# Kernel tuning notes

Hardware: AMD Instinct MI355X
Metric: run time of the kernel (lower is better)

The kernel has to match this reference:

```python
import jax, jax.numpy as jnp
import numpy as np

W_DIM = 512   # latent dim
CH = 512      # number of Fourier channels / output channels
SIZE = 64     # spatial size (square: size[0]=size[1])
SR = 64.0     # sampling_rate
BW = 2.0      # bandwidth
BATCH = 32


def setup_inputs() -> dict:
    key = jax.random.key(0)
    k1, k2, k3, k4, k5 = jax.random.split(key, 5)
    w = jax.random.normal(k1, (BATCH, W_DIM), jnp.float32)
    # affine FC params (weight_init=0 in original; use small random so t varies)
    affine_w = jax.random.normal(k2, (4, W_DIM), jnp.float32) * 0.1
    affine_b = jnp.array([1.0, 0.0, 0.0, 0.0], jnp.float32)
    # channel-mixing weight
    weight = jax.random.normal(k3, (CH, CH), jnp.float32)
    # freqs buffer init: randn, normalized by r*exp(r^2/4), scaled by bandwidth
    f = jax.random.normal(k4, (CH, 2), jnp.float32)
    radii = jnp.sqrt(jnp.sum(f * f, axis=1, keepdims=True))
    f = f / (radii * jnp.exp(radii * radii / 4.0)) * BW
    phases = jax.random.uniform(k5, (CH,), jnp.float32) - 0.5
    return {"w": w, "affine_w": affine_w, "affine_b": affine_b,
            "weight": weight, "freqs": f, "phases": phases}


def reference(w, affine_w, affine_b, weight, freqs, phases):
    # affine FC: FullyConnectedLayer with lr_multiplier=1 -> weight_gain = 1/sqrt(in)
    gain = np.float32(1.0 / np.sqrt(W_DIM))
    t = w @ (affine_w.T * gain) + affine_b                      # [N, 4]
    t = t / jnp.linalg.norm(t[:, :2], axis=1, keepdims=True)
    c, s, tx, ty = t[:, 0], t[:, 1], t[:, 2], t[:, 3]
    # combined transform = m_r @ m_t @ I; top-left 2x2 rotation block:
    R = jnp.stack([jnp.stack([c, -s], -1),
                   jnp.stack([s, c], -1)], axis=1)              # [N, 2, 2]
    # translation column of combined transform (m_r @ m_t)[:, :2, 2]
    trans = jnp.stack([-c * tx + s * ty, -s * tx - c * ty], -1) # [N, 2]
    ph = phases[None, :] + jnp.einsum('cd,nd->nc', freqs, trans)  # [N, C]
    fr = jnp.einsum('cd,nde->nce', freqs, R)                      # [N, C, 2]
    amp = jnp.clip(1.0 - (jnp.linalg.norm(fr, axis=2) - BW) / (SR / 2.0 - BW), 0.0, 1.0)  # [N, C]
    # affine_grid(theta, [1,1,H,W], align_corners=False): base coords (2i+1)/D - 1
    scale = np.float32(0.5 * SIZE / SR)
    xs = ((2.0 * jnp.arange(SIZE, dtype=jnp.float32) + 1.0) / SIZE - 1.0) * scale
    ys = ((2.0 * jnp.arange(SIZE, dtype=jnp.float32) + 1.0) / SIZE - 1.0) * scale
    grid = jnp.stack([jnp.broadcast_to(xs[None, :], (SIZE, SIZE)),
                      jnp.broadcast_to(ys[:, None], (SIZE, SIZE))], axis=-1)  # [H, W, 2]
    # per-pixel Fourier phase: [N, H, W, C]
    x = jnp.einsum('hwd,ncd->nhwc', grid, fr) + ph[:, None, None, :]
    x = jnp.sin(x * np.float32(2.0 * np.pi)) * amp[:, None, None, :]
    # channel projection, then to NCHW
    x = jnp.einsum('nhwc,kc->nkhw', x, weight * np.float32(1.0 / np.sqrt(CH)))
    return x  # [N, CH, H, W]
```

## Files before the change

### kernel.cpp

```cpp
#include <hip/hip_runtime.h>
#include <hip/hip_bf16.h>

#define WDIM 512
#define CHN  512
#define NB   32
#define SZ   64
#define MTOT 4096

typedef __attribute__((ext_vector_type(4))) float f32x4;
typedef __attribute__((ext_vector_type(8))) short short8;
typedef __attribute__((ext_vector_type(4))) int   int4v;
typedef __attribute__((ext_vector_type(4))) unsigned int uint4v;

__device__ __forceinline__ unsigned pack_bf(float a, float b) {
    union { __hip_bfloat16 h; unsigned short u; } x, y;
    x.h = __float2bfloat16(a); y.h = __float2bfloat16(b);
    return (unsigned)x.u | ((unsigned)y.u << 16);
}
__device__ __forceinline__ float lo16f(unsigned u) {
    union { unsigned x; float f; } t; t.x = u << 16; return t.f;
}
__device__ __forceinline__ float hi16f(unsigned u) {
    union { unsigned x; float f; } t; t.x = u & 0xffff0000u; return t.f;
}

__global__ __launch_bounds__(512) void prep_kernel(
    const float* __restrict__ win,
    const float* __restrict__ affine_w,
    const float* __restrict__ affine_b,
    const float* __restrict__ freqs,
    const float* __restrict__ phases,
    const float* __restrict__ wsrc,
    unsigned* __restrict__ SCA, unsigned* __restrict__ SCB,
    __hip_bfloat16* __restrict__ wbf)
{
    const int b = blockIdx.x;
    const int tid = threadIdx.x;
    if (b < NB * 64) {
        const int n = b >> 6;
        const int w = b & 63;
        __shared__ float red[8][4];
        __shared__ float par[4];

        float wv = win[n * WDIM + tid];
        float p0 = wv * affine_w[0 * WDIM + tid];
        float p1 = wv * affine_w[1 * WDIM + tid];
        float p2 = wv * affine_w[2 * WDIM + tid];
        float p3 = wv * affine_w[3 * WDIM + tid];
        #pragma unroll
        for (int off = 32; off >= 1; off >>= 1) {
            p0 += __shfl_down(p0, off);
            p1 += __shfl_down(p1, off);
            p2 += __shfl_down(p2, off);
            p3 += __shfl_down(p3, off);
        }
        const int wave = tid >> 6;
        if ((tid & 63) == 0) {
            red[wave][0] = p0; red[wave][1] = p1;
            red[wave][2] = p2; red[wave][3] = p3;
        }
        __syncthreads();
        if (tid == 0) {
            const float gain = 0.04419417382415922f;
            float t[4];
            #pragma unroll
            for (int j = 0; j < 4; ++j) {
                float s = 0.0f;
                #pragma unroll
                for (int v = 0; v < 8; ++v) s += red[v][j];
                t[j] = s * gain + affine_b[j];
            }
            float inv = 1.0f / sqrtf(t[0] * t[0] + t[1] * t[1]);
            float c = t[0] * inv, s = t[1] * inv, tx = t[2] * inv, ty = t[3] * inv;
            par[0] = c;
            par[1] = s;
            par[2] = -c * tx + s * ty;
            par[3] = -s * tx - c * ty;
        }
        __syncthreads();
        const float c_ = par[0], s_ = par[1], tr0 = par[2], tr1 = par[3];
        const int c = tid;
        float fx = freqs[c * 2 + 0], fy = freqs[c * 2 + 1];
        float frx = fx * c_ + fy * s_;
        float fry = -fx * s_ + fy * c_;
        float ph = phases[c] + fx * tr0 + fy * tr1;
        float r = sqrtf(frx * frx + fry * fry);
        float amp = 1.0f - (r - 2.0f) * (1.0f / 30.0f);
        amp = fminf(fmaxf(amp, 0.0f), 1.0f);
        float xs = (float)(2 * w + 1) * (1.0f / 128.0f) - 0.5f;
        size_t idx = ((size_t)(n * 64 + w)) * CHN + c;
        float sA = amp * __builtin_amdgcn_sinf(xs * frx);
        float cA = amp * __builtin_amdgcn_cosf(xs * frx);
        float bb = xs * fry + ph;
        SCA[idx] = pack_bf(sA, cA);
        SCB[idx] = pack_bf(__builtin_amdgcn_sinf(bb), __builtin_amdgcn_cosf(bb));
    } else {
        int i = (b - NB * 64) * 512 + tid;
        wbf[i] = __float2bfloat16(wsrc[i] * 0.04419417382415922f);
    }
}

__global__ __launch_bounds__(256, 2) void fused_kernel(
    const unsigned* __restrict__ SCA, const unsigned* __restrict__ SCB,
    const __hip_bfloat16* __restrict__ wbf,
    float* __restrict__ out)
{
    __shared__ __align__(16) __hip_bfloat16 As[128 * 64];
    __shared__ __align__(16) __hip_bfloat16 Bs[256 * 64];

    const int bid  = blockIdx.x;
    const int orig = (bid & 7) * 256 + (bid >> 3);
    const int n  = orig >> 6;
    const int kb = ((orig >> 5) & 1) * 256;
    const int mb = (orig & 31) * 128;
    const int h0 = mb >> 6;

    const int tid = threadIdx.x;
    const int lane = tid & 63;
    const int wid  = tid >> 6;
    const int ln15 = lane & 15;
    const int hi4  = lane >> 4;
    const int wk   = wid * 64;

    const int cc0 = (tid & 7) * 8;
    const int rb  = tid >> 3;

    const unsigned* pA0 = SCA + ((size_t)(n * 64 + rb)) * CHN + cc0;
    const unsigned* pA1 = pA0 + 32 * CHN;
    const unsigned* pB0 = SCB + ((size_t)(n * 64 + h0)) * CHN + cc0;
    const unsigned* pB1 = pB0 + CHN;

    f32x4 acc[4][8];
    #pragma unroll
    for (int a = 0; a < 4; ++a)
        #pragma unroll
        for (int b = 0; b < 8; ++b)
            acc[a][b] = (f32x4)0.0f;

    #pragma unroll 1
    for (int kc = 0; kc < 8; ++kc) {
        const int c0 = kc * 64;
        __syncthreads();

        #pragma unroll
        for (int u = 0; u < 8; ++u) {
            int unit = u * 256 + tid;
            int row = unit >> 3;
            int cbyte = ((unit & 7) << 4) ^ ((row & 7) << 4);
            const __hip_bfloat16* src = wbf + (size_t)(kb + row) * CHN + c0 + (cbyte >> 1);
            char* ldsbase = (char*)Bs + (u * 256 + (wid << 6)) * 16;
            __builtin_amdgcn_global_load_lds(
                (const __attribute__((address_space(1))) unsigned int*)src,
                (__attribute__((address_space(3))) unsigned int*)ldsbase, 16, 0, 0);
        }

        uint4v A00 = *(const uint4v*)(pA0 + c0), A01 = *(const uint4v*)(pA0 + c0 + 4);
        uint4v A10 = *(const uint4v*)(pA1 + c0), A11 = *(const uint4v*)(pA1 + c0 + 4);
        uint4v B00 = *(const uint4v*)(pB0 + c0), B01 = *(const uint4v*)(pB0 + c0 + 4);
        uint4v B10 = *(const uint4v*)(pB1 + c0), B11 = *(const uint4v*)(pB1 + c0 + 4);
        #pragma unroll
        for (int i = 0; i < 4; ++i) {
            int m = rb + i * 32;
            uint4v Aa = (i & 1) ? A10 : A00, Ab = (i & 1) ? A11 : A01;
            uint4v Ba = (i >> 1) ? B10 : B00, Bb = (i >> 1) ? B11 : B01;
            union { __hip_bfloat16 h[8]; int4v v; } t;
            #pragma unroll
            for (int j = 0; j < 4; ++j)
                t.h[j] = __float2bfloat16(
                    lo16f(Aa[j]) * hi16f(Ba[j]) + hi16f(Aa[j]) * lo16f(Ba[j]));
            #pragma unroll
            for (int j = 0; j < 4; ++j)
                t.h[4 + j] = __float2bfloat16(
                    lo16f(Ab[j]) * hi16f(Bb[j]) + hi16f(Ab[j]) * lo16f(Bb[j]));
            *(int4v*)((char*)As + m * 128 + ((cc0 * 2) ^ ((m & 7) << 4))) = t.v;
        }
        __syncthreads();

        #pragma unroll
        for (int kk = 0; kk < 2; ++kk) {
            short8 wf[4], ff[8];
            #pragma unroll
            for (int ki = 0; ki < 4; ++ki) {
                int row = wk + ki * 16 + ln15;
                wf[ki] = *(const short8*)((char*)Bs + row * 128 +
                          (((kk * 32 + hi4 * 8) * 2) ^ ((row & 7) << 4)));
            }
            #pragma unroll
            for (int mj = 0; mj < 8; ++mj) {
                int m = mj * 16 + ln15;
                ff[mj] = *(const short8*)((char*)As + m * 128 +
                          (((kk * 32 + hi4 * 8) * 2) ^ ((m & 7) << 4)));
            }
            __builtin_amdgcn_s_setprio(1);
            #pragma unroll
            for (int ki = 0; ki < 4; ++ki)
                #pragma unroll
                for (int mj = 0; mj < 8; ++mj)
                    acc[ki][mj] = __builtin_amdgcn_mfma_f32_16x16x32_bf16(
                        wf[ki], ff[mj], acc[ki][mj], 0, 0, 0);
            __builtin_amdgcn_s_setprio(0);
        }
    }

    #pragma unroll
    for (int ki = 0; ki < 4; ++ki) {
        #pragma unroll
        for (int mj = 0; mj < 8; ++mj) {
            int kg = kb + wk + ki * 16 + hi4 * 4;
            int mg = mb + mj * 16 + ln15;
            float* op = out + ((size_t)n * CHN + kg) * MTOT + mg;
            #pragma unroll
            for (int r = 0; r < 4; ++r)
                op[(size_t)r * MTOT] = acc[ki][mj][r];
        }
    }
}

extern "C" void kernel_launch(void* const* d_in, const int* in_sizes, int n_in,
                              void* d_out, int out_size, void* d_ws, size_t ws_size,
                              hipStream_t stream) {
    const float* w        = (const float*)d_in[0];
    const float* affine_w = (const float*)d_in[1];
    const float* affine_b = (const float*)d_in[2];
    const float* weight   = (const float*)d_in[3];
    const float* freqs    = (const float*)d_in[4];
    const float* phases   = (const float*)d_in[5];
    float* out = (float*)d_out;

    char* ws = (char*)d_ws;
    __hip_bfloat16* wbf = (__hip_bfloat16*)(ws);
    unsigned* SCA = (unsigned*)(ws + (1u << 20));
    unsigned* SCB = (unsigned*)(ws + (1u << 20) + (4u << 20));

    prep_kernel<<<NB * 64 + (CHN * CHN) / 512, 512, 0, stream>>>(
        w, affine_w, affine_b, freqs, phases, weight, SCA, SCB, wbf);

    fused_kernel<<<2048, 256, 0, stream>>>(SCA, SCB, wbf, out);
}
```

Before: 103.0 us.

## Warp-specialize fused GEMM into producer and consumer waves with double-buffered LDS

Result: slower. 121.1 us (+17.5%).

```diff
diff --git a/kernel.cpp b/kernel.cpp
--- a/kernel.cpp
+++ b/kernel.cpp
@@ -100,13 +100,13 @@
     }
 }
 
-__global__ __launch_bounds__(256, 2) void fused_kernel(
+__global__ __launch_bounds__(512, 2) void fused_kernel(
     const unsigned* __restrict__ SCA, const unsigned* __restrict__ SCB,
     const __hip_bfloat16* __restrict__ wbf,
     float* __restrict__ out)
 {
-    __shared__ __align__(16) __hip_bfloat16 As[128 * 64];
-    __shared__ __align__(16) __hip_bfloat16 Bs[256 * 64];
+    __shared__ __align__(16) __hip_bfloat16 As[2][128 * 64];
+    __shared__ __align__(16) __hip_bfloat16 Bs[2][256 * 64];
 
     const int bid  = blockIdx.x;
     const int orig = (bid & 7) * 256 + (bid >> 3);
@@ -116,102 +116,122 @@
     const int h0 = mb >> 6;
 
     const int tid = threadIdx.x;
-    const int lane = tid & 63;
-    const int wid  = tid >> 6;
-    const int ln15 = lane & 15;
-    const int hi4  = lane >> 4;
-    const int wk   = wid * 64;
-
-    const int cc0 = (tid & 7) * 8;
-    const int rb  = tid >> 3;
-
-    const unsigned* pA0 = SCA + ((size_t)(n * 64 + rb)) * CHN + cc0;
-    const unsigned* pA1 = pA0 + 32 * CHN;
-    const unsigned* pB0 = SCB + ((size_t)(n * 64 + h0)) * CHN + cc0;
-    const unsigned* pB1 = pB0 + CHN;
-
-    f32x4 acc[4][8];
-    #pragma unroll
-    for (int a = 0; a < 4; ++a)
+    const int wid = tid >> 6;
+    const bool producer = wid >= 4;
+
+    if (producer) {
+        const int ptid = tid - 256;
+        const int pwid = wid - 4;
+        const int cc0 = (ptid & 7) * 8;
+        const int rb  = ptid >> 3;
+
+        const unsigned* pA0 = SCA + ((size_t)(n * 64 + rb)) * CHN + cc0;
+        const unsigned* pA1 = pA0 + 32 * CHN;
+        const unsigned* pB0 = SCB + ((size_t)(n * 64 + h0)) * CHN + cc0;
+        const unsigned* pB1 = pB0 + CHN;
+
+        auto stageB = [&](int buf, int c0) {
+            #pragma unroll
+            for (int u = 0; u < 8; ++u) {
+                int unit = u * 256 + ptid;
+                int row = unit >> 3;
+                int cbyte = ((unit & 7) << 4) ^ ((row & 7) << 4);
+                const __hip_bfloat16* src = wbf + (size_t)(kb + row) * CHN + c0 + (cbyte >> 1);
+                char* ldsbase = (char*)Bs[buf] + (u * 256 + (pwid << 6)) * 16;
+                __builtin_amdgcn_global_load_lds(
+                    (const __attribute__((address_space(1))) unsigned int*)src,
+                    (__attribute__((address_space(3))) unsigned int*)ldsbase, 16, 0, 0);
+            }
+        };
+        auto features = [&](int buf, int c0) {
+            uint4v A00 = *(const uint4v*)(pA0 + c0), A01 = *(const uint4v*)(pA0 + c0 + 4);
+            uint4v A10 = *(const uint4v*)(pA1 + c0), A11 = *(const uint4v*)(pA1 + c0 + 4);
+            uint4v B00 = *(const uint4v*)(pB0 + c0), B01 = *(const uint4v*)(pB0 + c0 + 4);
+            uint4v B10 = *(const uint4v*)(pB1 + c0), B11 = *(const uint4v*)(pB1 + c0 + 4);
+            #pragma unroll
+            for (int i = 0; i < 4; ++i) {
+                int m = rb + i * 32;
+                uint4v Aa = (i & 1) ? A10 : A00, Ab = (i & 1) ? A11 : A01;
+                uint4v Ba = (i >> 1) ? B10 : B00, Bb = (i >> 1) ? B11 : B01;
+                union { __hip_bfloat16 h[8]; int4v v; } t;
+                #pragma unroll
+                for (int j = 0; j < 4; ++j)
+                    t.h[j] = __float2bfloat16(
+                        lo16f(Aa[j]) * hi16f(Ba[j]) + hi16f(Aa[j]) * lo16f(Ba[j]));
+                #pragma unroll
+                for (int j = 0; j < 4; ++j)
+                    t.h[4 + j] = __float2bfloat16(
+                        lo16f(Ab[j]) * hi16f(Bb[j]) + hi16f(Ab[j]) * lo16f(Bb[j]));
+                *(int4v*)((char*)As[buf] + m * 128 + ((cc0 * 2) ^ ((m & 7) << 4))) = t.v;
+            }
+        };
+
+        stageB(0, 0);
+        features(0, 0);
+        __syncthreads();
+        #pragma unroll 1
+        for (int kc = 0; kc < 8; ++kc) {
+            if (kc < 7) {
+                stageB((kc + 1) & 1, (kc + 1) * 64);
+                features((kc + 1) & 1, (kc + 1) * 64);
+            }
+            __syncthreads();
+        }
+    } else {
+        const int lane = tid & 63;
+        const int ln15 = lane & 15;
+        const int hi4  = lane >> 4;
+        const int wk   = wid * 64;
+
+        f32x4 acc[4][8];
         #pragma unroll
-        for (int b = 0; b < 8; ++b)
-            acc[a][b] = (f32x4)0.0f;
-
-    #pragma unroll 1
-    for (int kc = 0; kc < 8; ++kc) {
-        const int c0 = kc * 64;
-        __syncthreads();
+        for (int a = 0; a < 4; ++a)
+            #pragma unroll
+            for (int b = 0; b < 8; ++b)
+                acc[a][b] = (f32x4)0.0f;
+
+        __syncthreads();
+        #pragma unroll 1
+        for (int kc = 0; kc < 8; ++kc) {
+            const int buf = kc & 1;
+            #pragma unroll
+            for (int kk = 0; kk < 2; ++kk) {
+                short8 wf[4], ff[8];
+                #pragma unroll
+                for (int ki = 0; ki < 4; ++ki) {
+                    int row = wk + ki * 16 + ln15;
+                    wf[ki] = *(const short8*)((char*)Bs[buf] + row * 128 +
+                              (((kk * 32 + hi4 * 8) * 2) ^ ((row & 7) << 4)));
+                }
+                #pragma unroll
+                for (int mj = 0; mj < 8; ++mj) {
+                    int m = mj * 16 + ln15;
+                    ff[mj] = *(const short8*)((char*)As[buf] + m * 128 +
+                              (((kk * 32 + hi4 * 8) * 2) ^ ((m & 7) << 4)));
+                }
+                __builtin_amdgcn_s_setprio(1);
+                #pragma unroll
+                for (int ki = 0; ki < 4; ++ki)
+                    #pragma unroll
+                    for (int mj = 0; mj < 8; ++mj)
+                        acc[ki][mj] = __builtin_amdgcn_mfma_f32_16x16x32_bf16(
+                            wf[ki], ff[mj], acc[ki][mj], 0, 0, 0);
+                __builtin_amdgcn_s_setprio(0);
+            }
+            __syncthreads();
+        }
 
         #pragma unroll
-        for (int u = 0; u < 8; ++u) {
-            int unit = u * 256 + tid;
-            int row = unit >> 3;
-            int cbyte = ((unit & 7) << 4) ^ ((row & 7) << 4);
-            const __hip_bfloat16* src = wbf + (size_t)(kb + row) * CHN + c0 + (cbyte >> 1);
-            char* ldsbase = (char*)Bs + (u * 256 + (wid << 6)) * 16;
-            __builtin_amdgcn_global_load_lds(
-                (const __attribute__((address_space(1))) unsigned int*)src,
-                (__attribute__((address_space(3))) unsigned int*)ldsbase, 16, 0, 0);
-        }
-
-        uint4v A00 = *(const uint4v*)(pA0 + c0), A01 = *(const uint4v*)(pA0 + c0 + 4);
-        uint4v A10 = *(const uint4v*)(pA1 + c0), A11 = *(const uint4v*)(pA1 + c0 + 4);
-        uint4v B00 = *(const uint4v*)(pB0 + c0), B01 = *(const uint4v*)(pB0 + c0 + 4);
-        uint4v B10 = *(const uint4v*)(pB1 + c0), B11 = *(const uint4v*)(pB1 + c0 + 4);
-        #pragma unroll
-        for (int i = 0; i < 4; ++i) {
-            int m = rb + i * 32;
-            uint4v Aa = (i & 1) ? A10 : A00, Ab = (i & 1) ? A11 : A01;
-            uint4v Ba = (i >> 1) ? B10 : B00, Bb = (i >> 1) ? B11 : B01;
-            union { __hip_bfloat16 h[8]; int4v v; } t;
-            #pragma unroll
-            for (int j = 0; j < 4; ++j)
-                t.h[j] = __float2bfloat16(
-                    lo16f(Aa[j]) * hi16f(Ba[j]) + hi16f(Aa[j]) * lo16f(Ba[j]));
-            #pragma unroll
-            for (int j = 0; j < 4; ++j)
-                t.h[4 + j] = __float2bfloat16(
-                    lo16f(Ab[j]) * hi16f(Bb[j]) + hi16f(Ab[j]) * lo16f(Bb[j]));
-            *(int4v*)((char*)As + m * 128 + ((cc0 * 2) ^ ((m & 7) << 4))) = t.v;
-        }
-        __syncthreads();
-
-        #pragma unroll
-        for (int kk = 0; kk < 2; ++kk) {
-            short8 wf[4], ff[8];
-            #pragma unroll
-            for (int ki = 0; ki < 4; ++ki) {
-                int row = wk + ki * 16 + ln15;
-                wf[ki] = *(const short8*)((char*)Bs + row * 128 +
-                          (((kk * 32 + hi4 * 8) * 2) ^ ((row & 7) << 4)));
-            }
+        for (int ki = 0; ki < 4; ++ki) {
             #pragma unroll
             for (int mj = 0; mj < 8; ++mj) {
-                int m = mj * 16 + ln15;
-                ff[mj] = *(const short8*)((char*)As + m * 128 +
-                          (((kk * 32 + hi4 * 8) * 2) ^ ((m & 7) << 4)));
-            }
-            __builtin_amdgcn_s_setprio(1);
-            #pragma unroll
-            for (int ki = 0; ki < 4; ++ki)
-                #pragma unroll
-                for (int mj = 0; mj < 8; ++mj)
-                    acc[ki][mj] = __builtin_amdgcn_mfma_f32_16x16x32_bf16(
-                        wf[ki], ff[mj], acc[ki][mj], 0, 0, 0);
-            __builtin_amdgcn_s_setprio(0);
-        }
-    }
-
-    #pragma unroll
-    for (int ki = 0; ki < 4; ++ki) {
-        #pragma unroll
-        for (int mj = 0; mj < 8; ++mj) {
-            int kg = kb + wk + ki * 16 + hi4 * 4;
-            int mg = mb + mj * 16 + ln15;
-            float* op = out + ((size_t)n * CHN + kg) * MTOT + mg;
-            #pragma unroll
-            for (int r = 0; r < 4; ++r)
-                op[(size_t)r * MTOT] = acc[ki][mj][r];
+                int kg = kb + wk + ki * 16 + hi4 * 4;
+                int mg = mb + mj * 16 + ln15;
+                float* op = out + ((size_t)n * CHN + kg) * MTOT + mg;
+                #pragma unroll
+                for (int r = 0; r < 4; ++r)
+                    op[(size_t)r * MTOT] = acc[ki][mj][r];
+            }
         }
     }
 }
@@ -235,5 +255,5 @@
     prep_kernel<<<NB * 64 + (CHN * CHN) / 512, 512, 0, stream>>>(
         w, affine_w, affine_b, freqs, phases, weight, SCA, SCB, wbf);
 
-    fused_kernel<<<2048, 256, 0, stream>>>(SCA, SCB, wbf, out);
-}
+    fused_kernel<<<2048, 512, 0, stream>>>(SCA, SCB, wbf, out);
+}
```

## Load weights directly to registers and triple-buffer feature tiles in LDS

Applied to the files above, without the earlier changes.

Measured after the change: 127.7 us. 24.0% more time.

```diff
diff --git a/kernel.cpp b/kernel.cpp
--- a/kernel.cpp
+++ b/kernel.cpp
@@ -105,8 +105,7 @@
     const __hip_bfloat16* __restrict__ wbf,
     float* __restrict__ out)
 {
-    __shared__ __align__(16) __hip_bfloat16 As[128 * 64];
-    __shared__ __align__(16) __hip_bfloat16 Bs[256 * 64];
+    __shared__ __align__(16) __hip_bfloat16 As3[3][128 * 64];
 
     const int bid  = blockIdx.x;
     const int orig = (bid & 7) * 256 + (bid >> 3);
@@ -130,30 +129,18 @@
     const unsigned* pB0 = SCB + ((size_t)(n * 64 + h0)) * CHN + cc0;
     const unsigned* pB1 = pB0 + CHN;
 
-    f32x4 acc[4][8];
-    #pragma unroll
-    for (int a = 0; a < 4; ++a)
-        #pragma unroll
-        for (int b = 0; b < 8; ++b)
-            acc[a][b] = (f32x4)0.0f;
-
-    #pragma unroll 1
-    for (int kc = 0; kc < 8; ++kc) {
-        const int c0 = kc * 64;
-        __syncthreads();
-
-        #pragma unroll
-        for (int u = 0; u < 8; ++u) {
-            int unit = u * 256 + tid;
-            int row = unit >> 3;
-            int cbyte = ((unit & 7) << 4) ^ ((row & 7) << 4);
-            const __hip_bfloat16* src = wbf + (size_t)(kb + row) * CHN + c0 + (cbyte >> 1);
-            char* ldsbase = (char*)Bs + (u * 256 + (wid << 6)) * 16;
-            __builtin_amdgcn_global_load_lds(
-                (const __attribute__((address_space(1))) unsigned int*)src,
-                (__attribute__((address_space(3))) unsigned int*)ldsbase, 16, 0, 0);
-        }
-
+    const __hip_bfloat16* wrow = wbf + (size_t)(kb + wk + ln15) * CHN + hi4 * 8;
+
+    short8 wf[2][4][2];
+    auto loadW = [&](int pb, int c0) {
+        #pragma unroll
+        for (int ki = 0; ki < 4; ++ki)
+            #pragma unroll
+            for (int kk = 0; kk < 2; ++kk)
+                wf[pb][ki][kk] = *(const short8*)(wrow + (size_t)ki * 16 * CHN + c0 + kk * 32);
+    };
+
+    auto features = [&](int buf, int c0) {
         uint4v A00 = *(const uint4v*)(pA0 + c0), A01 = *(const uint4v*)(pA0 + c0 + 4);
         uint4v A10 = *(const uint4v*)(pA1 + c0), A11 = *(const uint4v*)(pA1 + c0 + 4);
         uint4v B00 = *(const uint4v*)(pB0 + c0), B01 = *(const uint4v*)(pB0 + c0 + 4);
@@ -172,23 +159,25 @@
             for (int j = 0; j < 4; ++j)
                 t.h[4 + j] = __float2bfloat16(
                     lo16f(Ab[j]) * hi16f(Bb[j]) + hi16f(Ab[j]) * lo16f(Bb[j]));
-            *(int4v*)((char*)As + m * 128 + ((cc0 * 2) ^ ((m & 7) << 4))) = t.v;
-        }
-        __syncthreads();
-
+            *(int4v*)((char*)As3[buf] + m * 128 + ((cc0 * 2) ^ ((m & 7) << 4))) = t.v;
+        }
+    };
+
+    f32x4 acc[4][8];
+    #pragma unroll
+    for (int a = 0; a < 4; ++a)
+        #pragma unroll
+        for (int b = 0; b < 8; ++b)
+            acc[a][b] = (f32x4)0.0f;
+
+    auto mfmaStep = [&](int pb, int buf) {
         #pragma unroll
         for (int kk = 0; kk < 2; ++kk) {
-            short8 wf[4], ff[8];
-            #pragma unroll
-            for (int ki = 0; ki < 4; ++ki) {
-                int row = wk + ki * 16 + ln15;
-                wf[ki] = *(const short8*)((char*)Bs + row * 128 +
-                          (((kk * 32 + hi4 * 8) * 2) ^ ((row & 7) << 4)));
-            }
+            short8 ff[8];
             #pragma unroll
             for (int mj = 0; mj < 8; ++mj) {
                 int m = mj * 16 + ln15;
-                ff[mj] = *(const short8*)((char*)As + m * 128 +
+                ff[mj] = *(const short8*)((char*)As3[buf] + m * 128 +
                           (((kk * 32 + hi4 * 8) * 2) ^ ((m & 7) << 4)));
             }
             __builtin_amdgcn_s_setprio(1);
@@ -197,9 +186,23 @@
                 #pragma unroll
                 for (int mj = 0; mj < 8; ++mj)
                     acc[ki][mj] = __builtin_amdgcn_mfma_f32_16x16x32_bf16(
-                        wf[ki], ff[mj], acc[ki][mj], 0, 0, 0);
+                        wf[pb][ki][kk], ff[mj], acc[ki][mj], 0, 0, 0);
             __builtin_amdgcn_s_setprio(0);
         }
+    };
+
+    features(0, 0);
+    __syncthreads();
+    loadW(0, 0);
+    features(1, 64);
+    __syncthreads();
+
+    #pragma unroll
+    for (int kc = 0; kc < 8; ++kc) {
+        if (kc < 7) loadW((kc + 1) & 1, (kc + 1) * 64);
+        mfmaStep(kc & 1, kc % 3);
+        if (kc < 6) features((kc + 2) % 3, (kc + 2) * 64);
+        __syncthreads();
     }
 
     #pragma unroll
```
